# Kernel tuning notes

Hardware: AMD Instinct MI355X
Metric: run time of the kernel (lower is better)

Reference implementation:

```python
import jax, jax.numpy as jnp
import numpy as np

B, L, V, D = 4096, 128, 50257, 64
NEG_INF = -1e9
COS_EPS = 1e-8  # torch cosine_similarity default eps


def setup_inputs() -> dict:
    key = jax.random.key(0)
    k1, k2, k3, k4, k5, k6 = jax.random.split(key, 6)
    return {
        "ids_a": jax.random.randint(k1, (B, L), 0, V, dtype=jnp.int64) if jax.config.jax_enable_x64 else jax.random.randint(k1, (B, L), 0, V, dtype=jnp.int32),
        "mask_a": jax.random.randint(k2, (B, L), 0, 2, dtype=jnp.int32),
        "ids_b": jax.random.randint(k3, (B, L), 0, V, dtype=jnp.int32),
        "mask_b": jax.random.randint(k4, (B, L), 0, 2, dtype=jnp.int32),
        "mu_table": jax.random.normal(k5, (V, D), dtype=jnp.float32),
        "feat_table": jax.random.normal(k6, (V, D), dtype=jnp.float32),
    }


def _side(ids, mask, mu_table, feat_table):
    # Embedding gathers: [B, L, D]
    mu = mu_table[ids]
    feat = feat_table[ids]
    m = mask.astype(mu.dtype)  # [B, L]
    # render_mean_pool: masked mean of mu -> query [B, D]
    denom = jnp.maximum(m.sum(axis=1, keepdims=True), 1.0)
    q = jnp.einsum('bld,bl->bd', mu, m) / denom
    # render_softmax_attention: single-query masked softmax over mu keys
    scores = jnp.einsum('bld,bd->bl', mu, q)
    scores = jnp.where(mask.astype(bool), scores, NEG_INF)
    attn = jax.nn.softmax(scores, axis=-1)  # [B, L]
    return jnp.einsum('bl,bld->bd', attn, feat)  # weighted sum of feat


def reference(ids_a, mask_a, ids_b, mask_b, mu_table, feat_table):
    mean_a = _side(ids_a, mask_a, mu_table, feat_table)
    mean_b = _side(ids_b, mask_b, mu_table, feat_table)
    # torch cosine_similarity: x.y / (max(||x||, eps) * max(||y||, eps))
    na = jnp.maximum(jnp.linalg.norm(mean_a, axis=-1), COS_EPS)
    nb = jnp.maximum(jnp.linalg.norm(mean_b, axis=-1), COS_EPS)
    cos = jnp.sum(mean_a * mean_b, axis=-1) / (na * nb)
    return cos * 5.0
```

## Files before the change

kernel.cpp:

```cpp
#include <hip/hip_runtime.h>
#include <math.h>

#define BB 4096
#define LL 128
#define DD 64

__global__ __launch_bounds__(256, 8) void softmax_attn_cos_kernel(
    const int* __restrict__ ids_a, const int* __restrict__ mask_a,
    const int* __restrict__ ids_b, const int* __restrict__ mask_b,
    const float* __restrict__ mu_table, const float* __restrict__ feat_table,
    float* __restrict__ out)
{
    __shared__ int    s_ids[2][LL];
    __shared__ float  s_msk[2][LL];
    __shared__ float4 s_q[2][16];
    __shared__ float4 s_qp[2][2][16];
    __shared__ float  s_sc[2][LL];
    __shared__ float4 s_op[2][2][16];
    __shared__ float  s_mean[2][DD];
    __shared__ float  s_sum[2];
    __shared__ int    s_nm[2];

    const int tid  = threadIdx.x;
    const int lane = tid & 63;
    const int wave = tid >> 6;
    const int side = wave >> 1;
    const int wsub = wave & 1;
    const int grp  = lane >> 4;
    const int c4   = lane & 15;
    const int b    = blockIdx.x;

    {
        const int si = tid >> 7;
        const int l  = tid & 127;
        const int* idp = si ? ids_b  : ids_a;
        const int* mp  = si ? mask_b : mask_a;
        s_ids[si][l] = idp[b * LL + l];
        s_msk[si][l] = (float)mp[b * LL + l];
    }
    __syncthreads();

    {
        float4 qp = make_float4(0.f, 0.f, 0.f, 0.f);
        #pragma unroll
        for (int it = 0; it < 16; ++it) {
            const int r = wsub * 64 + it * 4 + grp;
            if (s_msk[side][r] > 0.5f) {
                const float4 f =
                    ((const float4*)(mu_table + (size_t)s_ids[side][r] * DD))[c4];
                qp.x += f.x; qp.y += f.y; qp.z += f.z; qp.w += f.w;
            }
        }
        #pragma unroll
        for (int off = 16; off <= 32; off <<= 1) {
            qp.x += __shfl_xor(qp.x, off, 64);
            qp.y += __shfl_xor(qp.y, off, 64);
            qp.z += __shfl_xor(qp.z, off, 64);
            qp.w += __shfl_xor(qp.w, off, 64);
        }
        if (lane < 16) s_qp[side][wsub][c4] = qp;
    }
    __syncthreads();

    if (tid < 128) {
        const int si = tid >> 6;
        const int dd = tid & 63;
        float mv = s_msk[si][dd] + s_msk[si][dd + 64];
        #pragma unroll
        for (int off = 32; off; off >>= 1) mv += __shfl_xor(mv, off, 64);
        if (dd == 0) s_nm[si] = (int)(mv + 0.5f);
        const float denom = fmaxf(mv, 1.0f);
        if (dd < 16) {
            float4 q0 = s_qp[si][0][dd], q1 = s_qp[si][1][dd];
            float4 q;
            q.x = (q0.x + q1.x) / denom; q.y = (q0.y + q1.y) / denom;
            q.z = (q0.z + q1.z) / denom; q.w = (q0.w + q1.w) / denom;
            s_q[si][dd] = q;
        }
    }
    __syncthreads();

    {
        const float4 q4 = s_q[side][c4];
        #pragma unroll
        for (int it = 0; it < 16; ++it) {
            const int r = wsub * 64 + it * 4 + grp;
            float sc = -1e9f;
            if (s_msk[side][r] > 0.5f) {
                const float4 f =
                    ((const float4*)(mu_table + (size_t)s_ids[side][r] * DD))[c4];
                sc = f.x * q4.x + f.y * q4.y + f.z * q4.z + f.w * q4.w;
                #pragma unroll
                for (int off = 1; off <= 8; off <<= 1)
                    sc += __shfl_xor(sc, off, 64);
            }
            if (c4 == 0) s_sc[side][r] = sc;
        }
    }
    __syncthreads();

    if (wsub == 0) {
        const float s1 = s_sc[side][lane], s2 = s_sc[side][lane + 64];
        float mx = fmaxf(s1, s2);
        #pragma unroll
        for (int off = 32; off; off >>= 1) mx = fmaxf(mx, __shfl_xor(mx, off, 64));
        const float e1 = expf(s1 - mx), e2 = expf(s2 - mx);
        s_sc[side][lane] = e1; s_sc[side][lane + 64] = e2;
        float sm = e1 + e2;
        #pragma unroll
        for (int off = 32; off; off >>= 1) sm += __shfl_xor(sm, off, 64);
        if (lane == 0) s_sum[side] = sm;
    }
    __syncthreads();

    {
        const bool allm = (s_nm[side] == 0);
        float4 op = make_float4(0.f, 0.f, 0.f, 0.f);
        #pragma unroll
        for (int it = 0; it < 16; ++it) {
            const int r = wsub * 64 + it * 4 + grp;
            if (allm || s_msk[side][r] > 0.5f) {
                const float w = s_sc[side][r];
                const float4 f =
                    ((const float4*)(feat_table + (size_t)s_ids[side][r] * DD))[c4];
                op.x = fmaf(f.x, w, op.x); op.y = fmaf(f.y, w, op.y);
                op.z = fmaf(f.z, w, op.z); op.w = fmaf(f.w, w, op.w);
            }
        }
        #pragma unroll
        for (int off = 16; off <= 32; off <<= 1) {
            op.x += __shfl_xor(op.x, off, 64);
            op.y += __shfl_xor(op.y, off, 64);
            op.z += __shfl_xor(op.z, off, 64);
            op.w += __shfl_xor(op.w, off, 64);
        }
        if (lane < 16) s_op[side][wsub][c4] = op;
    }
    __syncthreads();

    if (tid < 32) {
        const int si = tid >> 4, cc = tid & 15;
        const float inv = 1.0f / s_sum[si];
        float4 o0 = s_op[si][0][cc], o1 = s_op[si][1][cc];
        float4 o;
        o.x = (o0.x + o1.x) * inv; o.y = (o0.y + o1.y) * inv;
        o.z = (o0.z + o1.z) * inv; o.w = (o0.w + o1.w) * inv;
        ((float4*)&s_mean[si][0])[cc] = o;
    }
    __syncthreads();

    if (tid < 64) {
        const float a = s_mean[0][tid], c = s_mean[1][tid];
        float dt = a * c, na = a * a, nb = c * c;
        #pragma unroll
        for (int off = 32; off; off >>= 1) {
            dt += __shfl_xor(dt, off, 64);
            na += __shfl_xor(na, off, 64);
            nb += __shfl_xor(nb, off, 64);
        }
        if (tid == 0) {
            const float denom = fmaxf(sqrtf(na), 1e-8f) * fmaxf(sqrtf(nb), 1e-8f);
            out[b] = 5.0f * dt / denom;
        }
    }
}

extern "C" void kernel_launch(void* const* d_in, const int* in_sizes, int n_in,
                              void* d_out, int out_size, void* d_ws, size_t ws_size,
                              hipStream_t stream) {
    const int*   ids_a  = (const int*)d_in[0];
    const int*   mask_a = (const int*)d_in[1];
    const int*   ids_b  = (const int*)d_in[2];
    const int*   mask_b = (const int*)d_in[3];
    const float* mu     = (const float*)d_in[4];
    const float* feat   = (const float*)d_in[5];
    float* out = (float*)d_out;

    softmax_attn_cos_kernel<<<BB, 256, 0, stream>>>(
        ids_a, mask_a, ids_b, mask_b, mu, feat, out);
}
```

Before: 130.5 us.

## Keep gathered mu rows in registers and prefetch feat rows before softmax

Each thread now keeps its 16 gathered mu float4 values in registers, so the scoring pass reuses them instead of gathering mu_table a second time. The feat_table gather is issued during the scoring loop, before the softmax barrier, so its latency overlaps the reductions and the weighted sum reads from registers. Holding 64 extra floats per thread raises register pressure, and the launch-bounds occupancy hint is cut from 8 to 4 blocks per CU to allow for it.

```diff
diff --git a/kernel.cpp b/kernel.cpp
--- a/kernel.cpp
+++ b/kernel.cpp
@@ -5,7 +5,7 @@
 #define LL 128
 #define DD 64
 
-__global__ __launch_bounds__(256, 8) void softmax_attn_cos_kernel(
+__global__ __launch_bounds__(256, 4) void softmax_attn_cos_kernel(
     const int* __restrict__ ids_a, const int* __restrict__ mask_a,
     const int* __restrict__ ids_b, const int* __restrict__ mask_b,
     const float* __restrict__ mu_table, const float* __restrict__ feat_table,
@@ -40,15 +40,18 @@
     }
     __syncthreads();
 
+    float4 v[16];
+    unsigned kept = 0;
     {
         float4 qp = make_float4(0.f, 0.f, 0.f, 0.f);
         #pragma unroll
         for (int it = 0; it < 16; ++it) {
             const int r = wsub * 64 + it * 4 + grp;
+            v[it] = make_float4(0.f, 0.f, 0.f, 0.f);
             if (s_msk[side][r] > 0.5f) {
-                const float4 f =
-                    ((const float4*)(mu_table + (size_t)s_ids[side][r] * DD))[c4];
-                qp.x += f.x; qp.y += f.y; qp.z += f.z; qp.w += f.w;
+                kept |= (1u << it);
+                v[it] = ((const float4*)(mu_table + (size_t)s_ids[side][r] * DD))[c4];
+                qp.x += v[it].x; qp.y += v[it].y; qp.z += v[it].z; qp.w += v[it].w;
             }
         }
         #pragma unroll
@@ -81,20 +84,21 @@
     __syncthreads();
 
     {
-        const float4 q4 = s_q[side][c4];
+        const float4 q4  = s_q[side][c4];
+        const bool  allm = (s_nm[side] == 0);
         #pragma unroll
         for (int it = 0; it < 16; ++it) {
             const int r = wsub * 64 + it * 4 + grp;
-            float sc = -1e9f;
-            if (s_msk[side][r] > 0.5f) {
-                const float4 f =
-                    ((const float4*)(mu_table + (size_t)s_ids[side][r] * DD))[c4];
-                sc = f.x * q4.x + f.y * q4.y + f.z * q4.z + f.w * q4.w;
-                #pragma unroll
-                for (int off = 1; off <= 8; off <<= 1)
-                    sc += __shfl_xor(sc, off, 64);
-            }
-            if (c4 == 0) s_sc[side][r] = sc;
+            const bool k = (kept >> it) & 1u;
+            float sc = v[it].x * q4.x + v[it].y * q4.y
+                     + v[it].z * q4.z + v[it].w * q4.w;
+            #pragma unroll
+            for (int off = 1; off <= 8; off <<= 1)
+                sc += __shfl_xor(sc, off, 64);
+            if (c4 == 0) s_sc[side][r] = k ? sc : -1e9f;
+            v[it] = make_float4(0.f, 0.f, 0.f, 0.f);
+            if (allm || k)
+                v[it] = ((const float4*)(feat_table + (size_t)s_ids[side][r] * DD))[c4];
         }
     }
     __syncthreads();
@@ -114,18 +118,13 @@
     __syncthreads();
 
     {
-        const bool allm = (s_nm[side] == 0);
         float4 op = make_float4(0.f, 0.f, 0.f, 0.f);
         #pragma unroll
         for (int it = 0; it < 16; ++it) {
             const int r = wsub * 64 + it * 4 + grp;
-            if (allm || s_msk[side][r] > 0.5f) {
-                const float w = s_sc[side][r];
-                const float4 f =
-                    ((const float4*)(feat_table + (size_t)s_ids[side][r] * DD))[c4];
-                op.x = fmaf(f.x, w, op.x); op.y = fmaf(f.y, w, op.y);
-                op.z = fmaf(f.z, w, op.z); op.w = fmaf(f.w, w, op.w);
-            }
+            const float w = s_sc[side][r];
+            op.x = fmaf(v[it].x, w, op.x); op.y = fmaf(v[it].y, w, op.y);
+            op.z = fmaf(v[it].z, w, op.z); op.w = fmaf(v[it].w, w, op.w);
         }
         #pragma unroll
         for (int off = 16; off <= 32; off <<= 1) {
```

Measured after the change: 129.4 us. Within noise of the previous version (-0.8%).

## Use one wavefront per side and replace block barriers with wave barriers

Applied to the files above, without the earlier changes.

Each side (a or b) is now handled by a single 64-lane wavefront instead of two. Each wave loops over all 128 tokens, so the cross-wave partial-sum exchanges and most __syncthreads calls go away, leaving one block barrier before the final cosine. The mask is packed into the sign bit of the id to cut shared-memory traffic. In exchange, each wave does twice as many serial gather iterations and the block shrinks to 128 threads, which lowers per-block parallelism and relies on more resident blocks to hide gather latency.

```diff
diff --git a/kernel.cpp b/kernel.cpp
--- a/kernel.cpp
+++ b/kernel.cpp
@@ -5,150 +5,114 @@
 #define LL 128
 #define DD 64
 
-__global__ __launch_bounds__(256, 8) void softmax_attn_cos_kernel(
+__global__ __launch_bounds__(128, 6) void softmax_attn_cos_kernel(
     const int* __restrict__ ids_a, const int* __restrict__ mask_a,
     const int* __restrict__ ids_b, const int* __restrict__ mask_b,
     const float* __restrict__ mu_table, const float* __restrict__ feat_table,
     float* __restrict__ out)
 {
-    __shared__ int    s_ids[2][LL];
-    __shared__ float  s_msk[2][LL];
-    __shared__ float4 s_q[2][16];
-    __shared__ float4 s_qp[2][2][16];
-    __shared__ float  s_sc[2][LL];
-    __shared__ float4 s_op[2][2][16];
-    __shared__ float  s_mean[2][DD];
-    __shared__ float  s_sum[2];
-    __shared__ int    s_nm[2];
+    __shared__ int   s_idm[2][LL];
+    __shared__ float s_sc[2][LL];
+    __shared__ float s_mean[2][DD];
 
     const int tid  = threadIdx.x;
     const int lane = tid & 63;
     const int wave = tid >> 6;
-    const int side = wave >> 1;
-    const int wsub = wave & 1;
     const int grp  = lane >> 4;
     const int c4   = lane & 15;
     const int b    = blockIdx.x;
 
-    {
-        const int si = tid >> 7;
-        const int l  = tid & 127;
-        const int* idp = si ? ids_b  : ids_a;
-        const int* mp  = si ? mask_b : mask_a;
-        s_ids[si][l] = idp[b * LL + l];
-        s_msk[si][l] = (float)mp[b * LL + l];
-    }
-    __syncthreads();
+    const int* idp = wave ? ids_b  : ids_a;
+    const int* mp  = wave ? mask_b : mask_a;
 
-    {
-        float4 qp = make_float4(0.f, 0.f, 0.f, 0.f);
-        #pragma unroll
-        for (int it = 0; it < 16; ++it) {
-            const int r = wsub * 64 + it * 4 + grp;
-            if (s_msk[side][r] > 0.5f) {
-                const float4 f =
-                    ((const float4*)(mu_table + (size_t)s_ids[side][r] * DD))[c4];
-                qp.x += f.x; qp.y += f.y; qp.z += f.z; qp.w += f.w;
-            }
-        }
-        #pragma unroll
-        for (int off = 16; off <= 32; off <<= 1) {
-            qp.x += __shfl_xor(qp.x, off, 64);
-            qp.y += __shfl_xor(qp.y, off, 64);
-            qp.z += __shfl_xor(qp.z, off, 64);
-            qp.w += __shfl_xor(qp.w, off, 64);
-        }
-        if (lane < 16) s_qp[side][wsub][c4] = qp;
-    }
-    __syncthreads();
+    const int id0 = idp[b * LL + lane];
+    const int id1 = idp[b * LL + lane + 64];
+    const int m0  = mp[b * LL + lane];
+    const int m1  = mp[b * LL + lane + 64];
+    s_idm[wave][lane]      = id0 | (m0 ? 0 : (int)0x80000000);
+    s_idm[wave][lane + 64] = id1 | (m1 ? 0 : (int)0x80000000);
+    __builtin_amdgcn_wave_barrier();
 
-    if (tid < 128) {
-        const int si = tid >> 6;
-        const int dd = tid & 63;
-        float mv = s_msk[si][dd] + s_msk[si][dd + 64];
-        #pragma unroll
-        for (int off = 32; off; off >>= 1) mv += __shfl_xor(mv, off, 64);
-        if (dd == 0) s_nm[si] = (int)(mv + 0.5f);
-        const float denom = fmaxf(mv, 1.0f);
-        if (dd < 16) {
-            float4 q0 = s_qp[si][0][dd], q1 = s_qp[si][1][dd];
-            float4 q;
-            q.x = (q0.x + q1.x) / denom; q.y = (q0.y + q1.y) / denom;
-            q.z = (q0.z + q1.z) / denom; q.w = (q0.w + q1.w) / denom;
-            s_q[si][dd] = q;
+    float mv = (float)(m0 + m1);
+    #pragma unroll
+    for (int off = 32; off; off >>= 1) mv += __shfl_xor(mv, off, 64);
+    const float denom = fmaxf(mv, 1.0f);
+    const bool  allm  = (mv < 0.5f);
+
+    float4 qp = make_float4(0.f, 0.f, 0.f, 0.f);
+    #pragma unroll
+    for (int it = 0; it < 32; ++it) {
+        const int im = s_idm[wave][it * 4 + grp];
+        if (im >= 0) {
+            const float4 f = ((const float4*)(mu_table + (size_t)im * DD))[c4];
+            qp.x += f.x; qp.y += f.y; qp.z += f.z; qp.w += f.w;
         }
     }
-    __syncthreads();
+    #pragma unroll
+    for (int off = 16; off <= 32; off <<= 1) {
+        qp.x += __shfl_xor(qp.x, off, 64);
+        qp.y += __shfl_xor(qp.y, off, 64);
+        qp.z += __shfl_xor(qp.z, off, 64);
+        qp.w += __shfl_xor(qp.w, off, 64);
+    }
+    const float rd = 1.0f / denom;
+    const float4 q4 = make_float4(qp.x * rd, qp.y * rd, qp.z * rd, qp.w * rd);
 
-    {
-        const float4 q4 = s_q[side][c4];
-        #pragma unroll
-        for (int it = 0; it < 16; ++it) {
-            const int r = wsub * 64 + it * 4 + grp;
-            float sc = -1e9f;
-            if (s_msk[side][r] > 0.5f) {
-                const float4 f =
-                    ((const float4*)(mu_table + (size_t)s_ids[side][r] * DD))[c4];
-                sc = f.x * q4.x + f.y * q4.y + f.z * q4.z + f.w * q4.w;
-                #pragma unroll
-                for (int off = 1; off <= 8; off <<= 1)
-                    sc += __shfl_xor(sc, off, 64);
-            }
-            if (c4 == 0) s_sc[side][r] = sc;
+    #pragma unroll
+    for (int it = 0; it < 32; ++it) {
+        const int r  = it * 4 + grp;
+        const int im = s_idm[wave][r];
+        float sc = -1e9f;
+        if (im >= 0) {
+            const float4 f = ((const float4*)(mu_table + (size_t)im * DD))[c4];
+            sc = f.x * q4.x + f.y * q4.y + f.z * q4.z + f.w * q4.w;
+            #pragma unroll
+            for (int off = 1; off <= 8; off <<= 1)
+                sc += __shfl_xor(sc, off, 64);
+        }
+        if (c4 == 0) s_sc[wave][r] = sc;
+    }
+    __builtin_amdgcn_wave_barrier();
+
+    const float s1 = s_sc[wave][lane], s2 = s_sc[wave][lane + 64];
+    float mx = fmaxf(s1, s2);
+    #pragma unroll
+    for (int off = 32; off; off >>= 1) mx = fmaxf(mx, __shfl_xor(mx, off, 64));
+    const float e1 = expf(s1 - mx), e2 = expf(s2 - mx);
+    s_sc[wave][lane] = e1; s_sc[wave][lane + 64] = e2;
+    __builtin_amdgcn_wave_barrier();
+    float sm = e1 + e2;
+    #pragma unroll
+    for (int off = 32; off; off >>= 1) sm += __shfl_xor(sm, off, 64);
+    const float inv = 1.0f / sm;
+
+    float4 op = make_float4(0.f, 0.f, 0.f, 0.f);
+    #pragma unroll
+    for (int it = 0; it < 32; ++it) {
+        const int r  = it * 4 + grp;
+        const int im = s_idm[wave][r];
+        if (allm || im >= 0) {
+            const int   id = im & 0x7fffffff;
+            const float w  = s_sc[wave][r];
+            const float4 f = ((const float4*)(feat_table + (size_t)id * DD))[c4];
+            op.x = fmaf(f.x, w, op.x); op.y = fmaf(f.y, w, op.y);
+            op.z = fmaf(f.z, w, op.z); op.w = fmaf(f.w, w, op.w);
         }
     }
+    #pragma unroll
+    for (int off = 16; off <= 32; off <<= 1) {
+        op.x += __shfl_xor(op.x, off, 64);
+        op.y += __shfl_xor(op.y, off, 64);
+        op.z += __shfl_xor(op.z, off, 64);
+        op.w += __shfl_xor(op.w, off, 64);
+    }
+    if (lane < 16) {
+        float4 o;
+        o.x = op.x * inv; o.y = op.y * inv; o.z = op.z * inv; o.w = op.w * inv;
+        ((float4*)&s_mean[wave][0])[c4] = o;
+    }
+
     __syncthreads();
-
-    if (wsub == 0) {
-        const float s1 = s_sc[side][lane], s2 = s_sc[side][lane + 64];
-        float mx = fmaxf(s1, s2);
-        #pragma unroll
-        for (int off = 32; off; off >>= 1) mx = fmaxf(mx, __shfl_xor(mx, off, 64));
-        const float e1 = expf(s1 - mx), e2 = expf(s2 - mx);
-        s_sc[side][lane] = e1; s_sc[side][lane + 64] = e2;
-        float sm = e1 + e2;
-        #pragma unroll
-        for (int off = 32; off; off >>= 1) sm += __shfl_xor(sm, off, 64);
-        if (lane == 0) s_sum[side] = sm;
-    }
-    __syncthreads();
-
-    {
-        const bool allm = (s_nm[side] == 0);
-        float4 op = make_float4(0.f, 0.f, 0.f, 0.f);
-        #pragma unroll
-        for (int it = 0; it < 16; ++it) {
-            const int r = wsub * 64 + it * 4 + grp;
-            if (allm || s_msk[side][r] > 0.5f) {
-                const float w = s_sc[side][r];
-                const float4 f =
-                    ((const float4*)(feat_table + (size_t)s_ids[side][r] * DD))[c4];
-                op.x = fmaf(f.x, w, op.x); op.y = fmaf(f.y, w, op.y);
-                op.z = fmaf(f.z, w, op.z); op.w = fmaf(f.w, w, op.w);
-            }
-        }
-        #pragma unroll
-        for (int off = 16; off <= 32; off <<= 1) {
-            op.x += __shfl_xor(op.x, off, 64);
-            op.y += __shfl_xor(op.y, off, 64);
-            op.z += __shfl_xor(op.z, off, 64);
-            op.w += __shfl_xor(op.w, off, 64);
-        }
-        if (lane < 16) s_op[side][wsub][c4] = op;
-    }
-    __syncthreads();
-
-    if (tid < 32) {
-        const int si = tid >> 4, cc = tid & 15;
-        const float inv = 1.0f / s_sum[si];
-        float4 o0 = s_op[si][0][cc], o1 = s_op[si][1][cc];
-        float4 o;
-        o.x = (o0.x + o1.x) * inv; o.y = (o0.y + o1.y) * inv;
-        o.z = (o0.z + o1.z) * inv; o.w = (o0.w + o1.w) * inv;
-        ((float4*)&s_mean[si][0])[cc] = o;
-    }
-    __syncthreads();
-
     if (tid < 64) {
         const float a = s_mean[0][tid], c = s_mean[1][tid];
         float dt = a * c, na = a * a, nb = c * c;
@@ -159,8 +123,8 @@
             nb += __shfl_xor(nb, off, 64);
         }
         if (tid == 0) {
-            const float denom = fmaxf(sqrtf(na), 1e-8f) * fmaxf(sqrtf(nb), 1e-8f);
-            out[b] = 5.0f * dt / denom;
+            const float dn = fmaxf(sqrtf(na), 1e-8f) * fmaxf(sqrtf(nb), 1e-8f);
+            out[b] = 5.0f * dt / dn;
         }
     }
 }
@@ -176,6 +140,6 @@
     const float* feat   = (const float*)d_in[5];
     float* out = (float*)d_out;
 
-    softmax_attn_cos_kernel<<<BB, 256, 0, stream>>>(
+    softmax_attn_cos_kernel<<<BB, 128, 0, stream>>>(
         ids_a, mask_a, ids_b, mask_b, mu, feat, out);
 }
```

After: 158.6 us. +21.5%, slower.

## Convert embedding tables to fp16 per call and gather half-precision rows

Applied to the files above, without the earlier changes.

Adds a preprocessing kernel that converts the mu and feature tables to fp16 in workspace on every call. The main kernel then gathers 128-byte half rows instead of 256-byte float rows, halving gather traffic. The cost is an extra full-table read and write per launch, plus reduced precision in the embeddings.

```diff
diff --git a/kernel.cpp b/kernel.cpp
--- a/kernel.cpp
+++ b/kernel.cpp
@@ -1,14 +1,44 @@
 #include <hip/hip_runtime.h>
+#include <hip/hip_fp16.h>
 #include <math.h>
 
 #define BB 4096
 #define LL 128
 #define DD 64
+#define VV 50257
+#define TAB_ELEMS (VV * DD)
+
+__global__ __launch_bounds__(256) void convert_tables_kernel(
+    const float* __restrict__ mu, const float* __restrict__ feat,
+    __half* __restrict__ out_mu, __half* __restrict__ out_feat)
+{
+    const int n4 = TAB_ELEMS / 4;
+    for (int i = blockIdx.x * blockDim.x + threadIdx.x; i < n4;
+         i += gridDim.x * blockDim.x) {
+        const float4 m = ((const float4*)mu)[i];
+        const float4 f = ((const float4*)feat)[i];
+        union { __half2 h[2]; uint2 u; } pm, pf;
+        pm.h[0] = __floats2half2_rn(m.x, m.y);
+        pm.h[1] = __floats2half2_rn(m.z, m.w);
+        pf.h[0] = __floats2half2_rn(f.x, f.y);
+        pf.h[1] = __floats2half2_rn(f.z, f.w);
+        ((uint2*)out_mu)[i]   = pm.u;
+        ((uint2*)out_feat)[i] = pf.u;
+    }
+}
+
+__device__ __forceinline__ float4 load_row4(const __half* __restrict__ tab,
+                                            int id, int c4) {
+    const uint2 raw = ((const uint2*)(tab + (size_t)id * DD))[c4];
+    const float2 f01 = __half22float2(*(const __half2*)&raw.x);
+    const float2 f23 = __half22float2(*(const __half2*)&raw.y);
+    return make_float4(f01.x, f01.y, f23.x, f23.y);
+}
 
 __global__ __launch_bounds__(256, 8) void softmax_attn_cos_kernel(
     const int* __restrict__ ids_a, const int* __restrict__ mask_a,
     const int* __restrict__ ids_b, const int* __restrict__ mask_b,
-    const float* __restrict__ mu_table, const float* __restrict__ feat_table,
+    const __half* __restrict__ mu_table, const __half* __restrict__ feat_table,
     float* __restrict__ out)
 {
     __shared__ int    s_ids[2][LL];
@@ -46,8 +76,7 @@
         for (int it = 0; it < 16; ++it) {
             const int r = wsub * 64 + it * 4 + grp;
             if (s_msk[side][r] > 0.5f) {
-                const float4 f =
-                    ((const float4*)(mu_table + (size_t)s_ids[side][r] * DD))[c4];
+                const float4 f = load_row4(mu_table, s_ids[side][r], c4);
                 qp.x += f.x; qp.y += f.y; qp.z += f.z; qp.w += f.w;
             }
         }
@@ -87,8 +116,7 @@
             const int r = wsub * 64 + it * 4 + grp;
             float sc = -1e9f;
             if (s_msk[side][r] > 0.5f) {
-                const float4 f =
-                    ((const float4*)(mu_table + (size_t)s_ids[side][r] * DD))[c4];
+                const float4 f = load_row4(mu_table, s_ids[side][r], c4);
                 sc = f.x * q4.x + f.y * q4.y + f.z * q4.z + f.w * q4.w;
                 #pragma unroll
                 for (int off = 1; off <= 8; off <<= 1)
@@ -120,9 +148,8 @@
         for (int it = 0; it < 16; ++it) {
             const int r = wsub * 64 + it * 4 + grp;
             if (allm || s_msk[side][r] > 0.5f) {
-                const float w = s_sc[side][r];
-                const float4 f =
-                    ((const float4*)(feat_table + (size_t)s_ids[side][r] * DD))[c4];
+                const float w  = s_sc[side][r];
+                const float4 f = load_row4(feat_table, s_ids[side][r], c4);
                 op.x = fmaf(f.x, w, op.x); op.y = fmaf(f.y, w, op.y);
                 op.z = fmaf(f.z, w, op.z); op.w = fmaf(f.w, w, op.w);
             }
@@ -176,6 +203,10 @@
     const float* feat   = (const float*)d_in[5];
     float* out = (float*)d_out;
 
+    __half* ws_mu   = (__half*)d_ws;
+    __half* ws_feat = ws_mu + TAB_ELEMS;
+
+    convert_tables_kernel<<<1024, 256, 0, stream>>>(mu, feat, ws_mu, ws_feat);
     softmax_attn_cos_kernel<<<BB, 256, 0, stream>>>(
-        ids_a, mask_a, ids_b, mask_b, mu, feat, out);
-}
+        ids_a, mask_a, ids_b, mask_b, ws_mu, ws_feat, out);
+}
```

After: 136.8 us. 1.05x slower.
